# Optimization experiments

Hardware: AMD Instinct MI355X
Metric: run time of the kernel (lower is better)

The kernel has to match this reference:

```python
import jax, jax.numpy as jnp
import numpy as np

B, LQ, LS, S = 64, 64, 512, 512
NEG = -1e6


def mask_for_lengths(lengths, max_len, mask_right=True):
    pos = jnp.arange(max_len)
    if mask_right:
        m = pos[None, :] >= lengths[:, None]
    else:
        m = pos[None, :] < lengths[:, None]
    return jnp.where(m, jnp.float32(NEG), jnp.float32(0.0))


def setup_inputs() -> dict:
    key = jax.random.key(0)
    ks = jax.random.split(key, 12)
    f = lambda k, shp: jax.random.normal(k, shp, jnp.float32)
    sc = np.float32(1.0 / np.sqrt(S))
    return {
        "encoded_question": f(ks[0], (B, LQ, S)),
        "encoded_support": f(ks[1], (B, LS, S)),
        "question_length": jax.random.randint(ks[2], (B,), 1, LQ + 1),
        "support_length": jax.random.randint(ks[3], (B,), LS // 2, LS + 1),
        "correct_start": jax.random.randint(ks[4], (B,), 0, LS),
        "answer2question": jnp.arange(B),
        "is_eval": 1,
        "W_qa": f(ks[5], (S, 1)) * sc,
        "W_qsi": f(ks[6], (S, S)) * sc,
        "b_qsi": jnp.zeros((S,), jnp.float32),
        "W_qs": f(ks[7], (2 * S, S)) * sc,
        "W_ss": f(ks[8], (S, 1)) * sc,
        "W_qei": f(ks[9], (S, S)) * sc,
        "b_qei": jnp.zeros((S,), jnp.float32),
        "W_qe": f(ks[10], (3 * S, S)) * sc,
        "W_es": f(ks[11], (S, 1)) * sc,
    }


def reference(encoded_question, encoded_support, question_length, support_length,
              correct_start, answer2question, is_eval,
              W_qa, W_qsi, b_qsi, W_qs, W_ss, W_qei, b_qei, W_qe, W_es):
    # question attention pooling
    att = jnp.einsum('bqd,do->bq', encoded_question, W_qa)
    att = att + mask_for_lengths(question_length, LQ)
    w = jax.nn.softmax(att, axis=1)                                   # [B,LQ]
    q_state = jnp.einsum('bqd,bq->bd', encoded_question, w)           # [B,S]

    # start scoring
    start_input = jnp.concatenate(
        [q_state[:, None, :] * encoded_support, encoded_support], axis=2)  # [B,LS,2S]
    q_start_inter = q_state @ W_qsi + b_qsi                           # [B,S]
    q_start_state = start_input @ W_qs + q_start_inter[:, None, :]    # [B,LS,S]
    support_mask = mask_for_lengths(support_length, LS)
    start_scores = jnp.einsum('bld,do->bl', jax.nn.relu(q_start_state), W_ss)
    start_scores = start_scores + support_mask                        # [B,LS]
    predicted_start_pointer = jnp.argmax(start_scores, axis=1)        # [B]

    # eval path: start_pointer = predicted argmax
    start_pointer = predicted_start_pointer
    u_s = jnp.take_along_axis(encoded_support,
                              start_pointer[:, None, None], axis=1)[:, 0, :]  # [B,S]

    # end scoring
    end_input = jnp.concatenate(
        [encoded_support * u_s[:, None, :], start_input], axis=2)     # [B,LS,3S]
    q_end_inter = q_state @ W_qei + b_qei
    q_end_state = end_input @ W_qe + q_end_inter[:, None, :]          # [B,LS,S]
    end_scores = jnp.einsum('bld,do->bl', jax.nn.relu(q_end_state), W_es)
    end_scores = end_scores + support_mask
    # eval: mask positions left of start_pointer
    end_scores = end_scores + mask_for_lengths(start_pointer, LS, mask_right=False)
    predicted_end_pointer = jnp.argmax(end_scores, axis=1)

    return (start_scores, end_scores, predicted_start_pointer, predicted_end_pointer)
```

## Files before the change

kernel.cpp:

```cpp
#include <hip/hip_runtime.h>
#include <math.h>

constexpr int B_  = 64;
constexpr int LQ_ = 64;
constexpr int LS_ = 512;
constexpr int S_  = 512;
#define NEGV (-1e6f)
#define MARGIN 0.0625f

typedef __attribute__((ext_vector_type(8))) short bf16x8;
typedef __attribute__((ext_vector_type(4))) float f32x4;

__device__ inline unsigned short f2bf_rn(float x) {
    unsigned u = __builtin_bit_cast(unsigned, x);
    unsigned r = (u + 0x7FFFu + ((u >> 16) & 1u)) >> 16;
    return (unsigned short)r;
}

__global__ __launch_bounds__(512)
void prep_support_kernel(const float* __restrict__ support, short* __restrict__ Aprep)
{
    int bid = blockIdx.x;
    int b = bid >> 3, rg = bid & 7;
    int t = threadIdx.x;
    int r  = t & 63;
    int cg = t >> 6;
    int row  = rg * 64 + r;
    int rc2  = row >> 8;
    int rowp = row & 255;
    const float* src = support + ((size_t)(b * LS_ + row)) * S_;

    #pragma unroll
    for (int ii = 0; ii < 2; ++ii) {
        int i = cg * 2 + ii;
        #pragma unroll
        for (int kc = 0; kc < 4; ++kc) {
            int d0 = i * 32 + kc * 8;
            float4 f0 = *(const float4*)(src + d0);
            float4 f1 = *(const float4*)(src + d0 + 4);
            uint4 H;
            H.x = f2bf_rn(f0.x) | ((unsigned)f2bf_rn(f0.y) << 16);
            H.y = f2bf_rn(f0.z) | ((unsigned)f2bf_rn(f0.w) << 16);
            H.z = f2bf_rn(f1.x) | ((unsigned)f2bf_rn(f1.y) << 16);
            H.w = f2bf_rn(f1.z) | ((unsigned)f2bf_rn(f1.w) << 16);
            size_t off = ((size_t)(b * 2 + rc2) * 16 + i) * 8192 + kc * 2048 + rowp * 8;
            *(uint4*)&Aprep[off] = H;
        }
    }
}

__global__ __launch_bounds__(256)
void qpool_kernel(const float* __restrict__ eq, const int* __restrict__ qlen,
                  const float* __restrict__ W_qa, float* __restrict__ q_state)
{
    int b = blockIdx.x;
    int t = threadIdx.x;
    int wave = t >> 6, lane = t & 63;
    __shared__ float att[LQ_];
    __shared__ float wsm[LQ_];
    const float* eqb = eq + (size_t)b * LQ_ * S_;

    for (int k = 0; k < 16; ++k) {
        int q = wave + 4 * k;
        const float* row = eqb + q * S_;
        float s = 0.f;
        #pragma unroll
        for (int j = 0; j < S_ / 64; ++j)
            s = fmaf(row[lane + 64 * j], W_qa[lane + 64 * j], s);
        #pragma unroll
        for (int off = 32; off >= 1; off >>= 1)
            s += __shfl_xor(s, off);
        if (lane == 0) att[q] = s;
    }
    __syncthreads();

    if (wave == 0) {
        int L = qlen[b];
        float v = att[lane] + ((lane < L) ? 0.f : NEGV);
        float m = v;
        #pragma unroll
        for (int off = 32; off >= 1; off >>= 1)
            m = fmaxf(m, __shfl_xor(m, off));
        float e = expf(v - m);
        float sum = e;
        #pragma unroll
        for (int off = 32; off >= 1; off >>= 1)
            sum += __shfl_xor(sum, off);
        wsm[lane] = e / sum;
    }
    __syncthreads();

    for (int d = t; d < S_; d += 256) {
        float acc = 0.f;
        #pragma unroll 8
        for (int q = 0; q < LQ_; ++q)
            acc = fmaf(wsm[q], eqb[q * S_ + d], acc);
        q_state[b * S_ + d] = acc;
    }
}

__global__ __launch_bounds__(512)
void inter_kernel(const float* __restrict__ q_state,
                  const float* __restrict__ W_qsi, const float* __restrict__ b_qsi,
                  const float* __restrict__ W_qei, const float* __restrict__ b_qei,
                  float* __restrict__ qsi, float* __restrict__ qei)
{
    int b = blockIdx.x;
    const float* W  = blockIdx.y ? W_qei : W_qsi;
    const float* bi = blockIdx.y ? b_qei : b_qsi;
    float*       o  = blockIdx.y ? qei   : qsi;
    int t = threadIdx.x, lane = t & 63, w = t >> 6;
    __shared__ float qs[S_];
    __shared__ float red[8][S_];
    qs[t] = q_state[b * S_ + t];
    __syncthreads();

    float z[8];
    #pragma unroll
    for (int k = 0; k < 8; ++k) z[k] = 0.f;
    const int d0 = w * 64;
    #pragma unroll 4
    for (int dd = 0; dd < 64; ++dd) {
        int d = d0 + dd;
        float q = qs[d];
        const float* row = W + (size_t)d * S_ + lane;
        #pragma unroll
        for (int k = 0; k < 8; ++k)
            z[k] = fmaf(q, row[k * 64], z[k]);
    }
    #pragma unroll
    for (int k = 0; k < 8; ++k) red[w][k * 64 + lane] = z[k];
    __syncthreads();
    float acc = bi[t];
    #pragma unroll
    for (int ww = 0; ww < 8; ++ww) acc += red[ww][t];
    o[b * S_ + t] = acc;
}

template <int NT>
__global__ __launch_bounds__(512)
void prep_kernel(const float* __restrict__ W, const float* __restrict__ q_state,
                 const float* __restrict__ u_s, short* __restrict__ Wc)
{
    int bid = blockIdx.x;
    int i = bid >> 6, b = bid & 63;
    int col = threadIdx.x;
    __shared__ float scq[32], scu[32];
    if (col < 32) scq[col] = q_state[b * S_ + i * 32 + col];
    if (NT == 3 && col >= 32 && col < 64) scu[col - 32] = u_s[b * S_ + i * 32 + col - 32];
    __syncthreads();

    unsigned short h[32];
    #pragma unroll
    for (int d = 0; d < 32; ++d) {
        int D = i * 32 + d;
        float v;
        if (NT == 2)
            v = fmaf(scq[d], W[(size_t)D * S_ + col], W[(size_t)(S_ + D) * S_ + col]);
        else
            v = fmaf(scu[d], W[(size_t)D * S_ + col],
                fmaf(scq[d], W[(size_t)(S_ + D) * S_ + col], W[(size_t)(2 * S_ + D) * S_ + col]));
        h[d] = f2bf_rn(v);
    }
    size_t base = ((size_t)b * 16 + i) * 16384 + (size_t)col * 8;
    #pragma unroll
    for (int kc = 0; kc < 4; ++kc) {
        uint4 H;
        H.x = h[kc*8+0] | ((unsigned)h[kc*8+1] << 16);
        H.y = h[kc*8+2] | ((unsigned)h[kc*8+3] << 16);
        H.z = h[kc*8+4] | ((unsigned)h[kc*8+5] << 16);
        H.w = h[kc*8+6] | ((unsigned)h[kc*8+7] << 16);
        *(uint4*)&Wc[base + kc * 4096] = H;
    }
}

template <bool END>
__global__ __launch_bounds__(512, 2)
void score_kernel(const short* __restrict__ Aprep, const short* __restrict__ Wc,
                  const float* __restrict__ inter, const float* __restrict__ Wsmall,
                  const int* __restrict__ slen, const int* __restrict__ sp,
                  float* __restrict__ out)
{
    const int t = threadIdx.x;
    const int lane = t & 63, wid = t >> 6;
    const int wr = wid >> 2, wc = wid & 3;
    const int l15 = lane & 15, l4 = lane >> 4;

    int lid = blockIdx.x;
    int xcd = lid & 7, slot = lid >> 3;
    int b  = xcd * 8 + (slot >> 2);
    int rc = slot & 3;
    int rc2 = rc >> 1, hh = rc & 1;

    __shared__ __attribute__((aligned(16))) short As[2][4096];
    __shared__ __attribute__((aligned(16))) short Bs[2][16384];
    __shared__ float int_l[S_], wsm_l[S_];
    __shared__ float sm_red[128][4];

    int_l[t] = inter[b * S_ + t];
    wsm_l[t] = Wsmall[t];

    const char* Abase = (const char*)(Aprep + ((size_t)(b * 2 + rc2) * 16) * 8192);
    const char* Bbase = (const char*)(Wc    + ((size_t)b * 16) * 16384);

    f32x4 acc[4][8];
    #pragma unroll
    for (int r = 0; r < 4; ++r)
        #pragma unroll
        for (int c = 0; c < 8; ++c)
            acc[r][c] = (f32x4){0.f, 0.f, 0.f, 0.f};

    const int akc = t >> 7, ar = t & 127;

    auto stage = [&](int i, int buf) {
        const char* ga = Abase + (size_t)i * 16384 + akc * 4096 + hh * 2048 + ar * 16;
        char* la = (char*)As[buf] + t * 16;
        __builtin_amdgcn_global_load_lds(
            (const __attribute__((address_space(1))) void*)ga,
            (__attribute__((address_space(3))) void*)la, 16, 0, 0);
        const char* gb = Bbase + (size_t)i * 32768 + t * 16;
        char* lb = (char*)Bs[buf] + t * 16;
        #pragma unroll
        for (int q = 0; q < 4; ++q)
            __builtin_amdgcn_global_load_lds(
                (const __attribute__((address_space(1))) void*)(gb + q * 8192),
                (__attribute__((address_space(3))) void*)(lb + q * 8192), 16, 0, 0);
    };

    stage(0, 0);

    for (int i = 0; i < 16; ++i) {
        const int buf = i & 1;
        if (i + 1 < 16) {
            stage(i + 1, buf ^ 1);
            asm volatile("s_waitcnt vmcnt(5)" ::: "memory");
        } else {
            asm volatile("s_waitcnt vmcnt(0)" ::: "memory");
        }
        __builtin_amdgcn_s_barrier();

        bf16x8 ah[4];
        #pragma unroll
        for (int r = 0; r < 4; ++r) {
            int rowp = wr * 64 + r * 16 + l15;
            ah[r] = *(const bf16x8*)&As[buf][l4 * 1024 + rowp * 8];
        }
        #pragma unroll
        for (int c = 0; c < 8; ++c) {
            int col = wc * 128 + c * 16 + l15;
            bf16x8 bh = *(const bf16x8*)&Bs[buf][l4 * 4096 + col * 8];
            #pragma unroll
            for (int r = 0; r < 4; ++r)
                acc[r][c] = __builtin_amdgcn_mfma_f32_16x16x32_bf16(ah[r], bh, acc[r][c], 0, 0, 0);
        }
        asm volatile("s_waitcnt lgkmcnt(0)" ::: "memory");
        __builtin_amdgcn_s_barrier();
    }

    #pragma unroll
    for (int r = 0; r < 4; ++r) {
        #pragma unroll
        for (int jj = 0; jj < 4; ++jj) {
            float pr = 0.f;
            #pragma unroll
            for (int c = 0; c < 8; ++c) {
                int col = wc * 128 + c * 16 + l15;
                float v = acc[r][c][jj] + int_l[col];
                v = fmaxf(v, 0.f);
                pr = fmaf(v, wsm_l[col], pr);
            }
            pr += __shfl_xor(pr, 1);
            pr += __shfl_xor(pr, 2);
            pr += __shfl_xor(pr, 4);
            pr += __shfl_xor(pr, 8);
            if (l15 == 0) sm_red[wr * 64 + r * 16 + l4 * 4 + jj][wc] = pr;
        }
    }
    __syncthreads();
    if (t < 128) {
        int l = rc * 128 + t;
        float s = sm_red[t][0] + sm_red[t][1] + sm_red[t][2] + sm_red[t][3];
        if (l >= slen[b]) s += NEGV;
        if (END) { if (l < sp[b]) s += NEGV; }
        out[b * LS_ + l] = s;
    }
}

__device__ inline int select_cands(const float* s_l, int t, int lane, int w,
                                   float* wred, int* wcnt, int* cand)
{
    float v = s_l[t];
    #pragma unroll
    for (int off = 32; off >= 1; off >>= 1)
        v = fmaxf(v, __shfl_xor(v, off));
    if (lane == 0) wred[w] = v;
    __syncthreads();
    float m = wred[0];
    #pragma unroll
    for (int k = 1; k < 8; ++k) m = fmaxf(m, wred[k]);
    float th = m - MARGIN;
    bool flag = s_l[t] >= th;
    unsigned long long bal = __ballot(flag);
    int rank = __popcll(bal & ((1ull << lane) - 1ull));
    if (lane == 0) wcnt[w] = (int)__popcll(bal);
    __syncthreads();
    int off = 0, total = 0;
    #pragma unroll
    for (int k = 0; k < 8; ++k) { if (k < w) off += wcnt[k]; total += wcnt[k]; }
    if (flag) { int pos = off + rank; if (pos < 8) cand[pos] = t; }
    __syncthreads();
    return total < 8 ? total : 8;
}

template <bool END>
__global__ __launch_bounds__(512)
void rescue_kernel(const float* __restrict__ support, const float* __restrict__ q_state,
                   const float* __restrict__ u_s_in, const float* __restrict__ Wbig,
                   const float* __restrict__ inter, const float* __restrict__ Wsmall,
                   const float* __restrict__ scores, float* __restrict__ part)
{
    int bid = blockIdx.x;
    int b = bid >> 3, cslot = bid & 7;
    int t = threadIdx.x, lane = t & 63, w = t >> 6;
    __shared__ float s_l[S_], qs_l[S_], us_l[S_], arow_sh[S_];
    __shared__ float red[8][S_];
    __shared__ float wred[8];
    __shared__ int wcnt[8], cand[8];

    s_l[t]  = scores[b * S_ + t];
    qs_l[t] = q_state[b * S_ + t];
    if (END) us_l[t] = u_s_in[b * S_ + t];
    __syncthreads();

    int cnt = select_cands(s_l, t, lane, w, wred, wcnt, cand);
    if (cnt == 1 || cslot >= cnt) return;

    int ci = cand[cslot];
    arow_sh[t] = support[((size_t)(b * LS_ + ci)) * S_ + t];
    __syncthreads();

    const float* W1 = Wbig;
    const float* W2 = Wbig + (size_t)S_ * S_;
    const float* W3 = Wbig + (size_t)2 * S_ * S_;
    const int d0 = w * 64;

    float z[8];
    #pragma unroll
    for (int j = 0; j < 8; ++j) z[j] = 0.f;

    #pragma unroll 2
    for (int dd = 0; dd < 64; ++dd) {
        int d = d0 + dd;
        float a  = arow_sh[d];
        float qa = qs_l[d] * a;
        float ua = END ? us_l[d] * a : 0.f;
        const float* r1 = W1 + (size_t)d * S_ + lane;
        const float* r2 = W2 + (size_t)d * S_ + lane;
        const float* r3 = W3 + (size_t)d * S_ + lane;
        #pragma unroll
        for (int j = 0; j < 8; ++j) {
            if (END)
                z[j] = fmaf(ua, r1[64 * j], fmaf(qa, r2[64 * j], fmaf(a, r3[64 * j], z[j])));
            else
                z[j] = fmaf(qa, r1[64 * j], fmaf(a, r2[64 * j], z[j]));
        }
    }
    #pragma unroll
    for (int j = 0; j < 8; ++j) red[w][lane + 64 * j] = z[j];
    __syncthreads();

    float v = 0.f;
    #pragma unroll
    for (int ww = 0; ww < 8; ++ww) v += red[ww][t];
    float p = fmaxf(v + inter[b * S_ + t], 0.f) * Wsmall[t];
    #pragma unroll
    for (int off = 32; off >= 1; off >>= 1)
        p += __shfl_xor(p, off);
    if (lane == 0) wred[w] = p;
    __syncthreads();
    if (t == 0) {
        float e = ((wred[0] + wred[1]) + (wred[2] + wred[3])) +
                  ((wred[4] + wred[5]) + (wred[6] + wred[7]));
        part[b * 8 + cslot] = e;
    }
}

template <bool END>
__global__ __launch_bounds__(512)
void finalize_kernel(const float* __restrict__ scores, const float* __restrict__ part,
                     const float* __restrict__ support, int* __restrict__ sp_ws,
                     float* __restrict__ pred, float* __restrict__ us_out)
{
    int b = blockIdx.x;
    int t = threadIdx.x, lane = t & 63, w = t >> 6;
    __shared__ float s_l[S_];
    __shared__ float wred[8];
    __shared__ int wcnt[8], cand[8];
    __shared__ int best_sh;

    s_l[t] = scores[b * S_ + t];
    __syncthreads();
    int cnt = select_cands(s_l, t, lane, w, wred, wcnt, cand);

    if (t == 0) {
        int bi = cand[0];
        if (cnt > 1) {
            float bv = -INFINITY;
            for (int c = 0; c < cnt; ++c) {
                float e = part[b * 8 + c];
                if (e > bv) { bv = e; bi = cand[c]; }
            }
        }
        best_sh = bi;
        pred[b] = (float)bi;
        if (!END) sp_ws[b] = bi;
    }
    __syncthreads();
    if (!END)
        us_out[b * S_ + t] = support[((size_t)(b * LS_ + best_sh)) * S_ + t];
}

extern "C" void kernel_launch(void* const* d_in, const int* in_sizes, int n_in,
                              void* d_out, int out_size, void* d_ws, size_t ws_size,
                              hipStream_t stream)
{
    const float* eq    = (const float*)d_in[0];
    const float* es    = (const float*)d_in[1];
    const int*   qlen  = (const int*)d_in[2];
    const int*   slen  = (const int*)d_in[3];
    const float* W_qa  = (const float*)d_in[7];
    const float* W_qsi = (const float*)d_in[8];
    const float* b_qsi = (const float*)d_in[9];
    const float* W_qs  = (const float*)d_in[10];
    const float* W_ss  = (const float*)d_in[11];
    const float* W_qei = (const float*)d_in[12];
    const float* b_qei = (const float*)d_in[13];
    const float* W_qe  = (const float*)d_in[14];
    const float* W_es  = (const float*)d_in[15];

    float* out          = (float*)d_out;
    float* start_scores = out;
    float* end_scores   = out + B_ * LS_;
    float* pred_start   = out + 2 * B_ * LS_;
    float* pred_end     = out + 2 * B_ * LS_ + B_;

    float* ws      = (float*)d_ws;
    float* q_state = ws;
    float* qsi     = ws + B_ * S_;
    float* qei     = ws + 2 * B_ * S_;
    float* u_s     = ws + 3 * B_ * S_;
    float* part    = ws + 4 * B_ * S_;
    int*   sp_ws   = (int*)(ws + 4 * B_ * S_ + 512);
    short* Wc      = (short*)(ws + 4 * B_ * S_ + 1024);
    short* Aprep   = Wc + (size_t)B_ * 16 * 16384;

    prep_support_kernel<<<512, 512, 0, stream>>>(es, Aprep);
    qpool_kernel<<<B_, 256, 0, stream>>>(eq, qlen, W_qa, q_state);
    inter_kernel<<<dim3(B_, 2), 512, 0, stream>>>(q_state, W_qsi, b_qsi, W_qei, b_qei, qsi, qei);

    prep_kernel<2><<<1024, 512, 0, stream>>>(W_qs, q_state, nullptr, Wc);
    score_kernel<false><<<256, 512, 0, stream>>>(Aprep, Wc, qsi, W_ss, slen, nullptr, start_scores);
    rescue_kernel<false><<<B_ * 8, 512, 0, stream>>>(es, q_state, nullptr, W_qs, qsi, W_ss,
                                                     start_scores, part);
    finalize_kernel<false><<<B_, 512, 0, stream>>>(start_scores, part, es, sp_ws, pred_start, u_s);

    prep_kernel<3><<<1024, 512, 0, stream>>>(W_qe, q_state, u_s, Wc);
    score_kernel<true><<<256, 512, 0, stream>>>(Aprep, Wc, qei, W_es, slen, sp_ws, end_scores);
    rescue_kernel<true><<<B_ * 8, 512, 0, stream>>>(es, q_state, u_s, W_qe, qei, W_es,
                                                    end_scores, part);
    finalize_kernel<true><<<B_, 512, 0, stream>>>(end_scores, part, es, nullptr, pred_end, nullptr);
}
```

Baseline: 193.3 us.

## Fuse support conversion and weight folding into score kernel, merge qpool with inter

Removes the separate support bf16 conversion and weight-folding prep kernels. The score kernel now loads fp32 support and weights directly, converts and folds them per k-step into shared memory, then runs MFMA. Question pooling is fused with the intermediate projection, so pooling is recomputed for each of the two projections. This removes intermediate global buffers and launches, but drops the double-buffered async LDS pipeline and recomputes the weight fold in each of the four row blocks per batch.

```diff
diff --git a/kernel.cpp b/kernel.cpp
--- a/kernel.cpp
+++ b/kernel.cpp
@@ -18,54 +18,31 @@
 }
 
 __global__ __launch_bounds__(512)
-void prep_support_kernel(const float* __restrict__ support, short* __restrict__ Aprep)
-{
-    int bid = blockIdx.x;
-    int b = bid >> 3, rg = bid & 7;
-    int t = threadIdx.x;
-    int r  = t & 63;
-    int cg = t >> 6;
-    int row  = rg * 64 + r;
-    int rc2  = row >> 8;
-    int rowp = row & 255;
-    const float* src = support + ((size_t)(b * LS_ + row)) * S_;
-
-    #pragma unroll
-    for (int ii = 0; ii < 2; ++ii) {
-        int i = cg * 2 + ii;
-        #pragma unroll
-        for (int kc = 0; kc < 4; ++kc) {
-            int d0 = i * 32 + kc * 8;
-            float4 f0 = *(const float4*)(src + d0);
-            float4 f1 = *(const float4*)(src + d0 + 4);
-            uint4 H;
-            H.x = f2bf_rn(f0.x) | ((unsigned)f2bf_rn(f0.y) << 16);
-            H.y = f2bf_rn(f0.z) | ((unsigned)f2bf_rn(f0.w) << 16);
-            H.z = f2bf_rn(f1.x) | ((unsigned)f2bf_rn(f1.y) << 16);
-            H.w = f2bf_rn(f1.z) | ((unsigned)f2bf_rn(f1.w) << 16);
-            size_t off = ((size_t)(b * 2 + rc2) * 16 + i) * 8192 + kc * 2048 + rowp * 8;
-            *(uint4*)&Aprep[off] = H;
-        }
-    }
-}
-
-__global__ __launch_bounds__(256)
-void qpool_kernel(const float* __restrict__ eq, const int* __restrict__ qlen,
-                  const float* __restrict__ W_qa, float* __restrict__ q_state)
+void qpool_inter_kernel(const float* __restrict__ eq, const int* __restrict__ qlen,
+                        const float* __restrict__ W_qa,
+                        const float* __restrict__ W_qsi, const float* __restrict__ b_qsi,
+                        const float* __restrict__ W_qei, const float* __restrict__ b_qei,
+                        float* __restrict__ q_state,
+                        float* __restrict__ qsi, float* __restrict__ qei)
 {
     int b = blockIdx.x;
-    int t = threadIdx.x;
-    int wave = t >> 6, lane = t & 63;
-    __shared__ float att[LQ_];
-    __shared__ float wsm[LQ_];
+    int which = blockIdx.y;
+    const float* W  = which ? W_qei : W_qsi;
+    const float* bi = which ? b_qei : b_qsi;
+    float*       o  = which ? qei   : qsi;
+
+    int t = threadIdx.x, lane = t & 63, w = t >> 6;
+    __shared__ float att[LQ_], wsm[LQ_], qs[S_];
+    __shared__ float red[8][S_];
     const float* eqb = eq + (size_t)b * LQ_ * S_;
 
-    for (int k = 0; k < 16; ++k) {
-        int q = wave + 4 * k;
+    #pragma unroll
+    for (int k = 0; k < 8; ++k) {
+        int q = w + 8 * k;
         const float* row = eqb + q * S_;
         float s = 0.f;
         #pragma unroll
-        for (int j = 0; j < S_ / 64; ++j)
+        for (int j = 0; j < 8; ++j)
             s = fmaf(row[lane + 64 * j], W_qa[lane + 64 * j], s);
         #pragma unroll
         for (int off = 32; off >= 1; off >>= 1)
@@ -74,7 +51,7 @@
     }
     __syncthreads();
 
-    if (wave == 0) {
+    if (w == 0) {
         int L = qlen[b];
         float v = att[lane] + ((lane < L) ? 0.f : NEGV);
         float m = v;
@@ -90,93 +67,46 @@
     }
     __syncthreads();
 
-    for (int d = t; d < S_; d += 256) {
+    {
         float acc = 0.f;
         #pragma unroll 8
         for (int q = 0; q < LQ_; ++q)
-            acc = fmaf(wsm[q], eqb[q * S_ + d], acc);
-        q_state[b * S_ + d] = acc;
-    }
-}
-
-__global__ __launch_bounds__(512)
-void inter_kernel(const float* __restrict__ q_state,
-                  const float* __restrict__ W_qsi, const float* __restrict__ b_qsi,
-                  const float* __restrict__ W_qei, const float* __restrict__ b_qei,
-                  float* __restrict__ qsi, float* __restrict__ qei)
-{
-    int b = blockIdx.x;
-    const float* W  = blockIdx.y ? W_qei : W_qsi;
-    const float* bi = blockIdx.y ? b_qei : b_qsi;
-    float*       o  = blockIdx.y ? qei   : qsi;
-    int t = threadIdx.x, lane = t & 63, w = t >> 6;
-    __shared__ float qs[S_];
-    __shared__ float red[8][S_];
-    qs[t] = q_state[b * S_ + t];
-    __syncthreads();
-
-    float z[8];
-    #pragma unroll
-    for (int k = 0; k < 8; ++k) z[k] = 0.f;
-    const int d0 = w * 64;
-    #pragma unroll 4
-    for (int dd = 0; dd < 64; ++dd) {
-        int d = d0 + dd;
-        float q = qs[d];
-        const float* row = W + (size_t)d * S_ + lane;
-        #pragma unroll
-        for (int k = 0; k < 8; ++k)
-            z[k] = fmaf(q, row[k * 64], z[k]);
-    }
-    #pragma unroll
-    for (int k = 0; k < 8; ++k) red[w][k * 64 + lane] = z[k];
-    __syncthreads();
-    float acc = bi[t];
-    #pragma unroll
-    for (int ww = 0; ww < 8; ++ww) acc += red[ww][t];
-    o[b * S_ + t] = acc;
+            acc = fmaf(wsm[q], eqb[q * S_ + t], acc);
+        qs[t] = acc;
+        if (which == 0) q_state[b * S_ + t] = acc;
+    }
+    __syncthreads();
+
+    {
+        float z[8];
+        #pragma unroll
+        for (int k = 0; k < 8; ++k) z[k] = 0.f;
+        const int d0 = w * 64;
+        #pragma unroll 4
+        for (int dd = 0; dd < 64; ++dd) {
+            int d = d0 + dd;
+            float q = qs[d];
+            const float* row = W + (size_t)d * S_ + lane;
+            #pragma unroll
+            for (int k = 0; k < 8; ++k)
+                z[k] = fmaf(q, row[k * 64], z[k]);
+        }
+        #pragma unroll
+        for (int k = 0; k < 8; ++k) red[w][k * 64 + lane] = z[k];
+    }
+    __syncthreads();
+    {
+        float acc = bi[t];
+        #pragma unroll
+        for (int ww = 0; ww < 8; ++ww) acc += red[ww][t];
+        o[b * S_ + t] = acc;
+    }
 }
 
 template <int NT>
 __global__ __launch_bounds__(512)
-void prep_kernel(const float* __restrict__ W, const float* __restrict__ q_state,
-                 const float* __restrict__ u_s, short* __restrict__ Wc)
-{
-    int bid = blockIdx.x;
-    int i = bid >> 6, b = bid & 63;
-    int col = threadIdx.x;
-    __shared__ float scq[32], scu[32];
-    if (col < 32) scq[col] = q_state[b * S_ + i * 32 + col];
-    if (NT == 3 && col >= 32 && col < 64) scu[col - 32] = u_s[b * S_ + i * 32 + col - 32];
-    __syncthreads();
-
-    unsigned short h[32];
-    #pragma unroll
-    for (int d = 0; d < 32; ++d) {
-        int D = i * 32 + d;
-        float v;
-        if (NT == 2)
-            v = fmaf(scq[d], W[(size_t)D * S_ + col], W[(size_t)(S_ + D) * S_ + col]);
-        else
-            v = fmaf(scu[d], W[(size_t)D * S_ + col],
-                fmaf(scq[d], W[(size_t)(S_ + D) * S_ + col], W[(size_t)(2 * S_ + D) * S_ + col]));
-        h[d] = f2bf_rn(v);
-    }
-    size_t base = ((size_t)b * 16 + i) * 16384 + (size_t)col * 8;
-    #pragma unroll
-    for (int kc = 0; kc < 4; ++kc) {
-        uint4 H;
-        H.x = h[kc*8+0] | ((unsigned)h[kc*8+1] << 16);
-        H.y = h[kc*8+2] | ((unsigned)h[kc*8+3] << 16);
-        H.z = h[kc*8+4] | ((unsigned)h[kc*8+5] << 16);
-        H.w = h[kc*8+6] | ((unsigned)h[kc*8+7] << 16);
-        *(uint4*)&Wc[base + kc * 4096] = H;
-    }
-}
-
-template <bool END>
-__global__ __launch_bounds__(512, 2)
-void score_kernel(const short* __restrict__ Aprep, const short* __restrict__ Wc,
+void score_kernel(const float* __restrict__ es, const float* __restrict__ q_state,
+                  const float* __restrict__ u_s, const float* __restrict__ Wbig,
                   const float* __restrict__ inter, const float* __restrict__ Wsmall,
                   const int* __restrict__ slen, const int* __restrict__ sp,
                   float* __restrict__ out)
@@ -190,18 +120,17 @@
     int xcd = lid & 7, slot = lid >> 3;
     int b  = xcd * 8 + (slot >> 2);
     int rc = slot & 3;
-    int rc2 = rc >> 1, hh = rc & 1;
-
-    __shared__ __attribute__((aligned(16))) short As[2][4096];
-    __shared__ __attribute__((aligned(16))) short Bs[2][16384];
-    __shared__ float int_l[S_], wsm_l[S_];
+
+    __shared__ __attribute__((aligned(16))) short As[4096];
+    __shared__ __attribute__((aligned(16))) short Bs[16384];
+    __shared__ float qs_l[S_], us_l[S_], int_l[S_], wsm_l[S_];
     __shared__ float sm_red[128][4];
 
+    qs_l[t]  = q_state[b * S_ + t];
     int_l[t] = inter[b * S_ + t];
     wsm_l[t] = Wsmall[t];
-
-    const char* Abase = (const char*)(Aprep + ((size_t)(b * 2 + rc2) * 16) * 8192);
-    const char* Bbase = (const char*)(Wc    + ((size_t)b * 16) * 16384);
+    if (NT == 3) us_l[t] = u_s[b * S_ + t];
+    __syncthreads();
 
     f32x4 acc[4][8];
     #pragma unroll
@@ -210,51 +139,65 @@
         for (int c = 0; c < 8; ++c)
             acc[r][c] = (f32x4){0.f, 0.f, 0.f, 0.f};
 
-    const int akc = t >> 7, ar = t & 127;
-
-    auto stage = [&](int i, int buf) {
-        const char* ga = Abase + (size_t)i * 16384 + akc * 4096 + hh * 2048 + ar * 16;
-        char* la = (char*)As[buf] + t * 16;
-        __builtin_amdgcn_global_load_lds(
-            (const __attribute__((address_space(1))) void*)ga,
-            (__attribute__((address_space(3))) void*)la, 16, 0, 0);
-        const char* gb = Bbase + (size_t)i * 32768 + t * 16;
-        char* lb = (char*)Bs[buf] + t * 16;
-        #pragma unroll
-        for (int q = 0; q < 4; ++q)
-            __builtin_amdgcn_global_load_lds(
-                (const __attribute__((address_space(1))) void*)(gb + q * 8192),
-                (__attribute__((address_space(3))) void*)(lb + q * 8192), 16, 0, 0);
-    };
-
-    stage(0, 0);
+    const int arow = t >> 2, akc = t & 3;
+    const float* aptr = es + ((size_t)(b * LS_ + rc * 128 + arow)) * S_ + akc * 8;
+    const float* W1 = Wbig;
+    const float* W2 = Wbig + (size_t)S_ * S_;
+    const float* W3 = Wbig + (size_t)2 * S_ * S_;
 
     for (int i = 0; i < 16; ++i) {
-        const int buf = i & 1;
-        if (i + 1 < 16) {
-            stage(i + 1, buf ^ 1);
-            asm volatile("s_waitcnt vmcnt(5)" ::: "memory");
-        } else {
-            asm volatile("s_waitcnt vmcnt(0)" ::: "memory");
-        }
-        __builtin_amdgcn_s_barrier();
+        const int k0 = i * 32;
+
+        float4 a0 = *(const float4*)(aptr + k0);
+        float4 a1 = *(const float4*)(aptr + k0 + 4);
+        uint4 HA;
+        HA.x = f2bf_rn(a0.x) | ((unsigned)f2bf_rn(a0.y) << 16);
+        HA.y = f2bf_rn(a0.z) | ((unsigned)f2bf_rn(a0.w) << 16);
+        HA.z = f2bf_rn(a1.x) | ((unsigned)f2bf_rn(a1.y) << 16);
+        HA.w = f2bf_rn(a1.z) | ((unsigned)f2bf_rn(a1.w) << 16);
+
+        uint4 HB[4];
+        #pragma unroll
+        for (int kc = 0; kc < 4; ++kc) {
+            unsigned short hv[8];
+            #pragma unroll
+            for (int e = 0; e < 8; ++e) {
+                int d = k0 + kc * 8 + e;
+                float v;
+                if (NT == 2)
+                    v = fmaf(qs_l[d], W1[(size_t)d * S_ + t], W2[(size_t)d * S_ + t]);
+                else
+                    v = fmaf(us_l[d], W1[(size_t)d * S_ + t],
+                        fmaf(qs_l[d], W2[(size_t)d * S_ + t], W3[(size_t)d * S_ + t]));
+                hv[e] = f2bf_rn(v);
+            }
+            HB[kc].x = hv[0] | ((unsigned)hv[1] << 16);
+            HB[kc].y = hv[2] | ((unsigned)hv[3] << 16);
+            HB[kc].z = hv[4] | ((unsigned)hv[5] << 16);
+            HB[kc].w = hv[6] | ((unsigned)hv[7] << 16);
+        }
+
+        __syncthreads();
+        *(uint4*)&As[akc * 1024 + arow * 8] = HA;
+        #pragma unroll
+        for (int kc = 0; kc < 4; ++kc)
+            *(uint4*)&Bs[kc * 4096 + t * 8] = HB[kc];
+        __syncthreads();
 
         bf16x8 ah[4];
         #pragma unroll
         for (int r = 0; r < 4; ++r) {
             int rowp = wr * 64 + r * 16 + l15;
-            ah[r] = *(const bf16x8*)&As[buf][l4 * 1024 + rowp * 8];
+            ah[r] = *(const bf16x8*)&As[l4 * 1024 + rowp * 8];
         }
         #pragma unroll
         for (int c = 0; c < 8; ++c) {
             int col = wc * 128 + c * 16 + l15;
-            bf16x8 bh = *(const bf16x8*)&Bs[buf][l4 * 4096 + col * 8];
+            bf16x8 bh = *(const bf16x8*)&Bs[l4 * 4096 + col * 8];
             #pragma unroll
             for (int r = 0; r < 4; ++r)
                 acc[r][c] = __builtin_amdgcn_mfma_f32_16x16x32_bf16(ah[r], bh, acc[r][c], 0, 0, 0);
         }
-        asm volatile("s_waitcnt lgkmcnt(0)" ::: "memory");
-        __builtin_amdgcn_s_barrier();
     }
 
     #pragma unroll
@@ -281,7 +224,7 @@
         int l = rc * 128 + t;
         float s = sm_red[t][0] + sm_red[t][1] + sm_red[t][2] + sm_red[t][3];
         if (l >= slen[b]) s += NEGV;
-        if (END) { if (l < sp[b]) s += NEGV; }
+        if (NT == 3) { if (l < sp[b]) s += NEGV; }
         out[b * LS_ + l] = s;
     }
 }
@@ -451,21 +394,18 @@
     float* u_s     = ws + 3 * B_ * S_;
     float* part    = ws + 4 * B_ * S_;
     int*   sp_ws   = (int*)(ws + 4 * B_ * S_ + 512);
-    short* Wc      = (short*)(ws + 4 * B_ * S_ + 1024);
-    short* Aprep   = Wc + (size_t)B_ * 16 * 16384;
-
-    prep_support_kernel<<<512, 512, 0, stream>>>(es, Aprep);
-    qpool_kernel<<<B_, 256, 0, stream>>>(eq, qlen, W_qa, q_state);
-    inter_kernel<<<dim3(B_, 2), 512, 0, stream>>>(q_state, W_qsi, b_qsi, W_qei, b_qei, qsi, qei);
-
-    prep_kernel<2><<<1024, 512, 0, stream>>>(W_qs, q_state, nullptr, Wc);
-    score_kernel<false><<<256, 512, 0, stream>>>(Aprep, Wc, qsi, W_ss, slen, nullptr, start_scores);
+
+    qpool_inter_kernel<<<dim3(B_, 2), 512, 0, stream>>>(
+        eq, qlen, W_qa, W_qsi, b_qsi, W_qei, b_qei, q_state, qsi, qei);
+
+    score_kernel<2><<<256, 512, 0, stream>>>(es, q_state, nullptr, W_qs, qsi, W_ss,
+                                             slen, nullptr, start_scores);
     rescue_kernel<false><<<B_ * 8, 512, 0, stream>>>(es, q_state, nullptr, W_qs, qsi, W_ss,
                                                      start_scores, part);
     finalize_kernel<false><<<B_, 512, 0, stream>>>(start_scores, part, es, sp_ws, pred_start, u_s);
 
-    prep_kernel<3><<<1024, 512, 0, stream>>>(W_qe, q_state, u_s, Wc);
-    score_kernel<true><<<256, 512, 0, stream>>>(Aprep, Wc, qei, W_es, slen, sp_ws, end_scores);
+    score_kernel<3><<<256, 512, 0, stream>>>(es, q_state, u_s, W_qe, qei, W_es,
+                                             slen, sp_ws, end_scores);
     rescue_kernel<true><<<B_ * 8, 512, 0, stream>>>(es, q_state, u_s, W_qe, qei, W_es,
                                                     end_scores, part);
     finalize_kernel<true><<<B_, 512, 0, stream>>>(end_scores, part, es, nullptr, pred_end, nullptr);
```

Result: slower. 263.7 us (+36.4%).
